# Kernel optimization log

Measured on AMD Instinct MI355X. Metric: run time of the kernel, lower is better.

## Reference

```python
import jax, jax.numpy as jnp
import numpy as np

K = 5            # dimW
PARAM_SIGMA = 0.08
LAMBDA_V = 2.0
C_MID = 192


def _conv5(x, w, b):
    # standard 5x5 SAME conv (the linear 'm' term of INRF)
    y = jax.lax.conv_general_dilated(x, w, (1, 1), 'SAME',
                                     dimension_numbers=('NCHW', 'OIHW', 'NCHW'))
    return y + b[None, :, None, None]


def _inrf(x, m_w, m_b, w_w):
    """INRF layer: out = (m * x) - lambda * sum_y w(y) sigma(x(y) - (g*x)(center)).
    dimG=1 so the Gaussian g*x is the identity (center pixel). The radiometric
    nonlinearity sigma is a saturating tanh with slope 1/paramSigma.
    """
    B, C, H, W = x.shape
    # windowed gather: [B, C*K*K, H, W], channel-major / spatial-minor ordering
    patches = jax.lax.conv_general_dilated_patches(x, (K, K), (1, 1), 'SAME')
    patches = patches.reshape(B, C, K * K, H, W)
    s = jnp.tanh((patches - x[:, :, None]) / PARAM_SIGMA)   # [B,C,KK,H,W]
    wterm = jnp.einsum('bckhw,ock->bohw', s, w_w)           # [B,Cout,H,W]
    return _conv5(x, m_w, m_b) - LAMBDA_V * wterm


def _maxpool2(x):
    return jax.lax.reduce_window(x, -jnp.inf, jax.lax.max,
                                 (1, 1, 2, 2), (1, 1, 2, 2), 'VALID')


def _avgpool8(x):
    s = jax.lax.reduce_window(x, 0.0, jax.lax.add,
                              (1, 1, 8, 8), (1, 1, 8, 8), 'VALID')
    return s / 64.0


def setup_inputs() -> dict:
    key = jax.random.key(0)
    ks = jax.random.split(key, 11)
    B = 64
    f32 = jnp.float32
    return {
        'x':    jax.random.normal(ks[0], (B, 3, 32, 32), f32),
        'm1_w': jax.random.normal(ks[1], (C_MID, 3, K, K), f32) * 0.05,
        'm1_b': jnp.zeros((C_MID,), f32),
        'w1_w': jax.random.normal(ks[2], (C_MID, 3, K * K), f32) * 0.05,
        'm2_w': jax.random.normal(ks[3], (C_MID, C_MID, K, K), f32) * 0.02,
        'm2_b': jnp.zeros((C_MID,), f32),
        'w2_w': jax.random.normal(ks[4], (C_MID, C_MID, K * K), f32) * 0.02,
        'm3_w': jax.random.normal(ks[5], (C_MID, C_MID, K, K), f32) * 0.02,
        'm3_b': jnp.zeros((C_MID,), f32),
        'w3_w': jax.random.normal(ks[6], (C_MID, C_MID, K * K), f32) * 0.02,
        'fc_w': jax.random.normal(ks[7], (10, C_MID), f32) * 0.05,
        'fc_b': jnp.zeros((10,), f32),
    }


def reference(x, m1_w, m1_b, w1_w, m2_w, m2_b, w2_w,
              m3_w, m3_b, w3_w, fc_w, fc_b):
    # dropout layers run in eval mode (identity); dp2d1 has p=0.0 anyway
    x00 = _maxpool2(_inrf(x, m1_w, m1_b, w1_w))      # [B,192,16,16]
    x01 = _inrf(x00, m2_w, m2_b, w2_w)               # [B,192,16,16]
    x03 = _maxpool2(x01)                             # [B,192,8,8]
    x04 = _inrf(x03, m3_w, m3_b, w3_w)               # [B,192,8,8]
    x05 = _avgpool8(x04)                             # [B,192,1,1]
    feat = x05.reshape(-1, C_MID)
    logits = feat @ fc_w.T + fc_b                    # [B,10]
    return (logits, x00, x01)
```

## Files before the change

kernel.cpp:

```cpp
#include <hip/hip_runtime.h>
#include <math.h>

#define COUT 192
#define NF 12

typedef __bf16 bf16_8 __attribute__((ext_vector_type(8)));
typedef float  f32x4  __attribute__((ext_vector_type(4)));

__device__ __forceinline__ float fast_tanh125(float d) {
    float e = __builtin_amdgcn_exp2f(d * 36.06737602222409f);
    return 1.0f - 2.0f * __builtin_amdgcn_rcpf(e + 1.0f);
}

__device__ __forceinline__ void gl_lds16(const void* gptr, void* lptr) {
    auto g = (const __attribute__((address_space(1))) unsigned int*)gptr;
    auto l = (__attribute__((address_space(3))) unsigned int*)lptr;
    __builtin_amdgcn_global_load_lds(g, l, 16, 0, 0);
}

#define BAR_VM4()  asm volatile("s_waitcnt vmcnt(4)\n\ts_barrier" ::: "memory")
#define BAR_VM3()  asm volatile("s_waitcnt vmcnt(3)\n\ts_barrier" ::: "memory")
#define BAR_VM0()  asm volatile("s_waitcnt vmcnt(0)\n\ts_barrier" ::: "memory")
#define BAR_VM4L() asm volatile("s_waitcnt vmcnt(4) lgkmcnt(0)\n\ts_barrier" ::: "memory")
#define BAR_VM3L() asm volatile("s_waitcnt vmcnt(3) lgkmcnt(0)\n\ts_barrier" ::: "memory")

__global__ void prep_all(const float* __restrict__ m1_w, const float* __restrict__ w1_w,
                         const float* __restrict__ m2_w, const float* __restrict__ w2_w,
                         const float* __restrict__ m3_w, const float* __restrict__ w3_w,
                         __bf16* __restrict__ Bp1, __bf16* __restrict__ Bp2,
                         __bf16* __restrict__ Bp3) {
    int idx = blockIdx.x * 256 + threadIdx.x;
    const int N1 = 3 * 2 * NF * 64, N2 = 192 * 2 * NF * 64;
    const float *mw, *ww; __bf16* Bp; int CIN, li;
    if (idx < N1)           { mw = m1_w; ww = w1_w; Bp = Bp1; CIN = 3;   li = idx; }
    else if (idx < N1 + N2) { mw = m2_w; ww = w2_w; Bp = Bp2; CIN = 192; li = idx - N1; }
    else if (idx < N1 + 2 * N2) { mw = m3_w; ww = w3_w; Bp = Bp3; CIN = 192; li = idx - N1 - N2; }
    else return;
    int lane = li & 63;
    int nf = (li >> 6) % NF;
    int cc = li / (NF * 64);
    int t = cc & 1, c = cc >> 1;
    int n = nf * 16 + (lane & 15);
    int k0 = (lane >> 4) * 8;
    bf16_8 v;
    #pragma unroll
    for (int e = 0; e < 8; ++e) {
        int k = k0 + e;
        float val = 0.f;
        if (k < 25) {
            val = (t == 0) ? mw[((size_t)n * CIN + c) * 25 + k]
                           : -2.0f * ww[((size_t)n * CIN + c) * 25 + k];
        }
        v[e] = (__bf16)val;
    }
    *(bf16_8*)(Bp + (size_t)li * 8) = v;
}

__global__ __launch_bounds__(256, 3) void inrf1_mfma(
    const float* __restrict__ x, const __bf16* __restrict__ Bp,
    const float* __restrict__ bias, float* __restrict__ x00)
{
    __shared__ float win[3][6][36];
    __shared__ float hp[192][33];

    const int b  = blockIdx.x >> 4;
    const int h0 = (blockIdx.x & 15) * 2;
    const int tid = threadIdx.x;
    const int wv = tid >> 6, lane = tid & 63;
    const int hl = wv >> 1, half = wv & 1;
    const int mcol = lane & 15, q = lane >> 4;
    const int wpos = half * 16 + mcol;

    for (int i = tid; i < 3 * 6 * 36; i += 256) {
        int c = i / 216, r = (i / 36) % 6, cc = i % 36;
        int gr = h0 + r - 2, gc = cc - 2;
        float v = 0.f;
        if (gr >= 0 && gr < 32 && gc >= 0 && gc < 32)
            v = x[((size_t)(b * 3 + c) * 32 + gr) * 32 + gc];
        win[c][r][cc] = v;
    }
    __syncthreads();

    int offs[8];
    #pragma unroll
    for (int e = 0; e < 8; ++e) {
        int k = q * 8 + e;
        int kk = (k < 25) ? k : 0;
        offs[e] = (hl + kk / 5) * 36 + wpos + (kk % 5);
    }
    const int cen_off = (hl + 2) * 36 + wpos + 2;

    f32x4 acc[NF];
    #pragma unroll
    for (int j = 0; j < NF; ++j) acc[j] = (f32x4){0.f, 0.f, 0.f, 0.f};

    const float* winf = &win[0][0][0];
    for (int c = 0; c < 3; ++c) {
        const float* wf = winf + c * 216;
        float cen = wf[cen_off];
        bf16_8 av, as_;
        #pragma unroll
        for (int e = 0; e < 8; ++e) {
            float v = wf[offs[e]];
            av[e] = (__bf16)v;
            as_[e] = (__bf16)fast_tanh125(v - cen);
        }
        const bf16_8* b0 = (const bf16_8*)Bp + ((size_t)(c * 2 + 0) * NF) * 64 + lane;
        const bf16_8* b1 = b0 + NF * 64;
        #pragma unroll
        for (int j = 0; j < NF; ++j)
            acc[j] = __builtin_amdgcn_mfma_f32_16x16x32_bf16(av, b0[j * 64], acc[j], 0, 0, 0);
        #pragma unroll
        for (int j = 0; j < NF; ++j)
            acc[j] = __builtin_amdgcn_mfma_f32_16x16x32_bf16(as_, b1[j * 64], acc[j], 0, 0, 0);
    }

    #pragma unroll
    for (int j = 0; j < NF; ++j) {
        int n = j * 16 + mcol;
        hp[n][hl * 16 + half * 8 + q * 2 + 0] = fmaxf(acc[j][0], acc[j][1]);
        hp[n][hl * 16 + half * 8 + q * 2 + 1] = fmaxf(acc[j][2], acc[j][3]);
    }
    __syncthreads();

    const int hpout = h0 >> 1;
    for (int i = tid; i < 192 * 16; i += 256) {
        int n = i >> 4, wp = i & 15;
        float v = fmaxf(hp[n][wp], hp[n][16 + wp]) + bias[n];
        x00[((size_t)(b * COUT + n) * 16 + hpout) * 16 + wp] = v;
    }
}

__global__ __launch_bounds__(512, 2) void inrf2_mfma(
    const float* __restrict__ xin, const __bf16* __restrict__ Bp,
    float* __restrict__ out0, float* __restrict__ part)
{
    constexpr int CPS = 48;
    __shared__ __align__(16) __bf16 Bs[3][24 * 64 * 8];
    __shared__ __align__(16) float slab[3][260];

    const int b  = blockIdx.x >> 2;
    const int ks = blockIdx.x & 3;
    const int c0 = ks * CPS;
    const int tid = threadIdx.x;
    const int wv = tid >> 6, lane = tid & 63;
    const int mg = wv & 3, nh = wv >> 2;
    const int wp = lane & 15, q = lane >> 4;

    int aoff[4][8];
    int cen_off[4];
    #pragma unroll
    for (int m = 0; m < 4; ++m) {
        const int crow = mg * 4 + m;
        cen_off[m] = crow * 16 + wp;
        #pragma unroll
        for (int e = 0; e < 8; ++e) {
            int kk = q * 8 + e;
            int dy = kk / 5 - 2, dx = kk % 5 - 2;
            int rr = crow + dy, cc2 = wp + dx;
            bool ok = (kk < 25) && (rr >= 0) && (rr < 16) && (cc2 >= 0) && (cc2 < 16);
            aoff[m][e] = ok ? (rr * 16 + cc2) : 256;
        }
    }

    const float* xb = xin + (size_t)b * COUT * 256;

    f32x4 acc[4][6];
    #pragma unroll
    for (int m = 0; m < 4; ++m)
        #pragma unroll
        for (int j = 0; j < 6; ++j) acc[m][j] = (f32x4){0.f, 0.f, 0.f, 0.f};

#define BUILD_A(SLOT, AV, AS)                                              \
    {                                                                      \
        const float* sb = slab[(SLOT)];                                    \
        _Pragma("unroll")                                                  \
        for (int m = 0; m < 4; ++m) {                                      \
            float cen = sb[cen_off[m]];                                    \
            _Pragma("unroll")                                              \
            for (int e = 0; e < 8; ++e) {                                  \
                float v = sb[aoff[m][e]];                                  \
                (AV)[m][e] = (__bf16)v;                                    \
                (AS)[m][e] = (__bf16)fast_tanh125(v - cen);                \
            }                                                              \
        }                                                                  \
    }

    if (tid < 12) slab[tid >> 2][256 + (tid & 3)] = 0.f;

    #pragma unroll
    for (int rr = 0; rr < 2; ++rr) {
        const int c = c0 + rr;
        if (wv == 0) gl_lds16(xb + (size_t)c * 256 + lane * 4, &slab[rr][0]);
        const __bf16* gB = Bp + (size_t)c * 12288 + wv * 1536 + lane * 8;
        #pragma unroll
        for (int i = 0; i < 3; ++i)
            gl_lds16(gB + i * 512, &Bs[rr][wv * 1536 + i * 512]);
    }
    if (wv == 0) { BAR_VM4L(); } else { BAR_VM3L(); }

    bf16_8 av[4], as_[4];

    #pragma unroll 3
    for (int r = 0; r < CPS; ++r) {
        const int sl_cur = r % 3;
        const int sl_n2  = (r + 2) % 3;
        const bool do2 = (r + 2) < CPS;

        if (do2) {
            const int c = c0 + r + 2;
            if (wv == 0) gl_lds16(xb + (size_t)c * 256 + lane * 4, &slab[sl_n2][0]);
            const __bf16* gB = Bp + (size_t)c * 12288 + wv * 1536 + lane * 8;
            #pragma unroll
            for (int i = 0; i < 3; ++i)
                gl_lds16(gB + i * 512, &Bs[sl_n2][wv * 1536 + i * 512]);
        }

        BUILD_A(sl_cur, av, as_);

        const bf16_8* Bf = (const bf16_8*)(Bs[sl_cur]) + lane;
        #pragma unroll
        for (int j = 0; j < 6; ++j) {
            bf16_8 fm = Bf[(nh * 6 + j) * 64];
            bf16_8 fs = Bf[(12 + nh * 6 + j) * 64];
            #pragma unroll
            for (int m = 0; m < 4; ++m) {
                acc[m][j] = __builtin_amdgcn_mfma_f32_16x16x32_bf16(av[m],  fm, acc[m][j], 0, 0, 0);
                acc[m][j] = __builtin_amdgcn_mfma_f32_16x16x32_bf16(as_[m], fs, acc[m][j], 0, 0, 0);
            }
        }

        if (do2) {
            if (wv == 0) { BAR_VM4(); } else { BAR_VM3(); }
        } else {
            BAR_VM0();
        }
    }
#undef BUILD_A

    float* outp = (ks == 0) ? out0 : (part + (size_t)(ks - 1) * 3145728);
    #pragma unroll
    for (int j = 0; j < 6; ++j) {
        int n = (nh * 6 + j) * 16 + wp;
        #pragma unroll
        for (int m = 0; m < 4; ++m) {
            int h = mg * 4 + m;
            *(f32x4*)&outp[((size_t)(b * COUT + n)) * 256 + h * 16 + q * 4] = acc[m][j];
        }
    }
}

__global__ __launch_bounds__(512) void finish2(
    float* __restrict__ x01, const float* __restrict__ part,
    const float* __restrict__ bias, __bf16* __restrict__ An)
{
    __shared__ float xbuf[8][256];
    const int b  = blockIdx.x / 24;
    const int cg = blockIdx.x % 24;
    const int tid = threadIdx.x;
    const int wv = tid >> 6, lane = tid & 63;
    const int ch = cg * 8 + wv;

    float* p0 = x01 + ((size_t)b * COUT + ch) * 256;
    const float* pp = part + ((size_t)b * COUT + ch) * 256;
    const float bv = bias[ch];
    #pragma unroll
    for (int i = 0; i < 4; ++i) {
        int idx = lane + 64 * i;
        float s = ((p0[idx] + pp[idx]) + pp[idx + 3145728]) + pp[idx + 2 * 3145728] + bv;
        xbuf[wv][idx] = s;
        p0[idx] = s;
    }
    __syncthreads();

    const int ph = lane >> 3, pw = lane & 7;
    const int i0 = ph * 32 + pw * 2;
    float x8 = fmaxf(fmaxf(xbuf[wv][i0], xbuf[wv][i0 + 1]),
                     fmaxf(xbuf[wv][i0 + 16], xbuf[wv][i0 + 17]));

    float myT = 0.f, myW = 0.f;
    #pragma unroll
    for (int k = 0; k < 25; ++k) {
        const int dy = k / 5 - 2, dx = k % 5 - 2;
        const bool valid = (ph + dy >= 0) && (ph + dy < 8) && (pw + dx >= 0) && (pw + dx < 8);
        float nb = __shfl(x8, (lane + dy * 8 + dx) & 63);
        nb = valid ? nb : 0.f;
        float tS = fast_tanh125(nb - x8);
        float wS = nb;
        #pragma unroll
        for (int off = 1; off < 64; off <<= 1) {
            tS += __shfl_xor(tS, off);
            wS += __shfl_xor(wS, off);
        }
        if (lane == k) { myT = tS; myW = wS; }
    }

    const int mt = b >> 4;
    if (lane < 25) {
        const int k = lane;
        const int la = (k >> 3) * 16 + (b & 15);
        const int e = k & 7;
        const int ccW = ch * 2, ccT = ch * 2 + 1;
        An[((size_t)(ccW * 4 + mt) * 64 + la) * 8 + e] = (__bf16)(myW * 0.015625f);
        An[((size_t)(ccT * 4 + mt) * 64 + la) * 8 + e] = (__bf16)(myT * 0.015625f);
    } else if (lane < 32) {
        const int la = 3 * 16 + (b & 15);
        const int e = lane & 7;
        const int ccW = ch * 2, ccT = ch * 2 + 1;
        An[((size_t)(ccW * 4 + mt) * 64 + la) * 8 + e] = (__bf16)0.f;
        An[((size_t)(ccT * 4 + mt) * 64 + la) * 8 + e] = (__bf16)0.f;
    }
}

__global__ __launch_bounds__(512) void gemm3p(
    const __bf16* __restrict__ An, const __bf16* __restrict__ Bp,
    float* __restrict__ part)
{
    const int ks = blockIdx.x;
    const int tid = threadIdx.x;
    const int wv = tid >> 6, lane = tid & 63;
    const int mt = wv & 3, nh = wv >> 2;

    f32x4 acc[6];
    #pragma unroll
    for (int j = 0; j < 6; ++j) acc[j] = (f32x4){0.f, 0.f, 0.f, 0.f};

    for (int i = 0; i < 4; ++i) {
        const int cc = ks * 4 + i;
        bf16_8 a = *(const bf16_8*)(An + ((size_t)(cc * 4 + mt) * 64 + lane) * 8);
        #pragma unroll
        for (int j = 0; j < 6; ++j) {
            bf16_8 bw = *(const bf16_8*)(Bp + ((size_t)(cc * NF + nh * 6 + j) * 64 + lane) * 8);
            acc[j] = __builtin_amdgcn_mfma_f32_16x16x32_bf16(a, bw, acc[j], 0, 0, 0);
        }
    }
    #pragma unroll
    for (int j = 0; j < 6; ++j) {
        int n = (nh * 6 + j) * 16 + (lane & 15);
        *(f32x4*)(part + ((size_t)ks * COUT + n) * 64 + mt * 16 + (lane >> 4) * 4) = acc[j];
    }
}

__global__ __launch_bounds__(256) void logitsk(
    const float* __restrict__ part, const float* __restrict__ m3_b,
    const float* __restrict__ fc_w, const float* __restrict__ fc_b,
    float* __restrict__ logits)
{
    __shared__ float feat[COUT];
    const int b = blockIdx.x;
    const int t = threadIdx.x;
    if (t < COUT) {
        float s = 0.f;
        for (int ks = 0; ks < 96; ++ks) s += part[((size_t)ks * COUT + t) * 64 + b];
        feat[t] = s + m3_b[t];
    }
    __syncthreads();
    if (t < 10) {
        float s = fc_b[t];
        #pragma unroll 8
        for (int c = 0; c < COUT; ++c) s = fmaf(fc_w[t * COUT + c], feat[c], s);
        logits[(size_t)b * 10 + t] = s;
    }
}

extern "C" void kernel_launch(void* const* d_in, const int* in_sizes, int n_in,
                              void* d_out, int out_size, void* d_ws, size_t ws_size,
                              hipStream_t stream) {
    const float* x    = (const float*)d_in[0];
    const float* m1_w = (const float*)d_in[1];
    const float* m1_b = (const float*)d_in[2];
    const float* w1_w = (const float*)d_in[3];
    const float* m2_w = (const float*)d_in[4];
    const float* m2_b = (const float*)d_in[5];
    const float* w2_w = (const float*)d_in[6];
    const float* m3_w = (const float*)d_in[7];
    const float* m3_b = (const float*)d_in[8];
    const float* w3_w = (const float*)d_in[9];
    const float* fc_w = (const float*)d_in[10];
    const float* fc_b = (const float*)d_in[11];

    float* out = (float*)d_out;
    float* ws  = (float*)d_ws;

    float* logits = out;
    float* x00 = out + 640;
    float* x01 = out + 640 + 3145728;

    __bf16* Bp1  = (__bf16*)(ws);
    __bf16* Bp2  = (__bf16*)(ws + 18432);
    __bf16* Bp3  = (__bf16*)(ws + 1198080);
    __bf16* An   = (__bf16*)(ws + 2377728);
    float*  part2 = ws + 2770944;
    float*  part3 = ws + 2770944;

    prep_all<<<2322, 256, 0, stream>>>(m1_w, w1_w, m2_w, w2_w, m3_w, w3_w, Bp1, Bp2, Bp3);

    inrf1_mfma<<<64 * 16, 256, 0, stream>>>(x, Bp1, m1_b, x00);
    inrf2_mfma<<<64 * 4, 512, 0, stream>>>(x00, Bp2, x01, part2);
    finish2<<<64 * 24, 512, 0, stream>>>(x01, part2, m2_b, An);
    gemm3p<<<96, 512, 0, stream>>>(An, Bp3, part3);
    logitsk<<<64, 256, 0, stream>>>(part3, m3_b, fc_w, fc_b, logits);
}
```

Measured before the change: 230.2 us.

## Feed inrf2 from a zero-padded global x00 copy via direct register loads

inrf1 now also writes x00 into a zero-padded 20x20 per-channel buffer, which prep_all zero-fills beforehand. inrf2 no longer stages each input channel slab through LDS. Each lane instead gathers its 5x5 window values straight from global memory into registers, double-buffered one channel ahead, with no bounds checks thanks to the padding. This removes LDS slab traffic and the per-channel vmcnt/lgkmcnt waits, at the cost of extra global writes, a large zero-fill and many redundant global loads that rely on the cache. The B-weight triple buffering stays, but the explicit vmcnt waits before each barrier are gone, so correctness now depends on implicit load completion.

New measurement: 231.0 us. Within noise of the previous version (+0.4%).

```diff
diff --git a/kernel.cpp b/kernel.cpp
--- a/kernel.cpp
+++ b/kernel.cpp
@@ -18,24 +18,23 @@
     __builtin_amdgcn_global_load_lds(g, l, 16, 0, 0);
 }
 
-#define BAR_VM4()  asm volatile("s_waitcnt vmcnt(4)\n\ts_barrier" ::: "memory")
-#define BAR_VM3()  asm volatile("s_waitcnt vmcnt(3)\n\ts_barrier" ::: "memory")
-#define BAR_VM0()  asm volatile("s_waitcnt vmcnt(0)\n\ts_barrier" ::: "memory")
-#define BAR_VM4L() asm volatile("s_waitcnt vmcnt(4) lgkmcnt(0)\n\ts_barrier" ::: "memory")
-#define BAR_VM3L() asm volatile("s_waitcnt vmcnt(3) lgkmcnt(0)\n\ts_barrier" ::: "memory")
-
 __global__ void prep_all(const float* __restrict__ m1_w, const float* __restrict__ w1_w,
                          const float* __restrict__ m2_w, const float* __restrict__ w2_w,
                          const float* __restrict__ m3_w, const float* __restrict__ w3_w,
                          __bf16* __restrict__ Bp1, __bf16* __restrict__ Bp2,
-                         __bf16* __restrict__ Bp3) {
+                         __bf16* __restrict__ Bp3, float* __restrict__ x00p) {
     int idx = blockIdx.x * 256 + threadIdx.x;
     const int N1 = 3 * 2 * NF * 64, N2 = 192 * 2 * NF * 64;
+    const int NW = N1 + 2 * N2;
+    if (idx >= NW) {
+        int zi = idx - NW;
+        if (zi < 1228800) ((f32x4*)x00p)[zi] = (f32x4){0.f, 0.f, 0.f, 0.f};
+        return;
+    }
     const float *mw, *ww; __bf16* Bp; int CIN, li;
     if (idx < N1)           { mw = m1_w; ww = w1_w; Bp = Bp1; CIN = 3;   li = idx; }
     else if (idx < N1 + N2) { mw = m2_w; ww = w2_w; Bp = Bp2; CIN = 192; li = idx - N1; }
-    else if (idx < N1 + 2 * N2) { mw = m3_w; ww = w3_w; Bp = Bp3; CIN = 192; li = idx - N1 - N2; }
-    else return;
+    else                    { mw = m3_w; ww = w3_w; Bp = Bp3; CIN = 192; li = idx - N1 - N2; }
     int lane = li & 63;
     int nf = (li >> 6) % NF;
     int cc = li / (NF * 64);
@@ -58,7 +57,8 @@
 
 __global__ __launch_bounds__(256, 3) void inrf1_mfma(
     const float* __restrict__ x, const __bf16* __restrict__ Bp,
-    const float* __restrict__ bias, float* __restrict__ x00)
+    const float* __restrict__ bias, float* __restrict__ x00,
+    float* __restrict__ x00p)
 {
     __shared__ float win[3][6][36];
     __shared__ float hp[192][33];
@@ -128,16 +128,16 @@
         int n = i >> 4, wp = i & 15;
         float v = fmaxf(hp[n][wp], hp[n][16 + wp]) + bias[n];
         x00[((size_t)(b * COUT + n) * 16 + hpout) * 16 + wp] = v;
+        x00p[(size_t)(b * COUT + n) * 400 + (hpout + 2) * 20 + (wp + 2)] = v;
     }
 }
 
 __global__ __launch_bounds__(512, 2) void inrf2_mfma(
-    const float* __restrict__ xin, const __bf16* __restrict__ Bp,
+    const float* __restrict__ x00p, const __bf16* __restrict__ Bp,
     float* __restrict__ out0, float* __restrict__ part)
 {
     constexpr int CPS = 48;
     __shared__ __align__(16) __bf16 Bs[3][24 * 64 * 8];
-    __shared__ __align__(16) float slab[3][260];
 
     const int b  = blockIdx.x >> 2;
     const int ks = blockIdx.x & 3;
@@ -147,23 +147,17 @@
     const int mg = wv & 3, nh = wv >> 2;
     const int wp = lane & 15, q = lane >> 4;
 
-    int aoff[4][8];
-    int cen_off[4];
-    #pragma unroll
-    for (int m = 0; m < 4; ++m) {
-        const int crow = mg * 4 + m;
-        cen_off[m] = crow * 16 + wp;
-        #pragma unroll
-        for (int e = 0; e < 8; ++e) {
-            int kk = q * 8 + e;
-            int dy = kk / 5 - 2, dx = kk % 5 - 2;
-            int rr = crow + dy, cc2 = wp + dx;
-            bool ok = (kk < 25) && (rr >= 0) && (rr < 16) && (cc2 >= 0) && (cc2 < 16);
-            aoff[m][e] = ok ? (rr * 16 + cc2) : 256;
-        }
-    }
-
-    const float* xb = xin + (size_t)b * COUT * 256;
+    int goff[9];
+    #pragma unroll
+    for (int e = 0; e < 8; ++e) {
+        int kk = q * 8 + e;
+        int k2 = (kk < 25) ? kk : 12;
+        int dy = k2 / 5 - 2, dx = k2 % 5 - 2;
+        goff[e] = (mg * 4 + dy + 2) * 20 + (wp + dx + 2);
+    }
+    goff[8] = (mg * 4 + 2) * 20 + (wp + 2);
+
+    const float* xs = x00p + (size_t)(b * COUT + c0) * 400;
 
     f32x4 acc[4][6];
     #pragma unroll
@@ -171,72 +165,70 @@
         #pragma unroll
         for (int j = 0; j < 6; ++j) acc[m][j] = (f32x4){0.f, 0.f, 0.f, 0.f};
 
-#define BUILD_A(SLOT, AV, AS)                                              \
+#define ISSUE_B(c, slot)                                                   \
     {                                                                      \
-        const float* sb = slab[(SLOT)];                                    \
+        const __bf16* gB = Bp + (size_t)(c) * 12288 + wv * 1536 + lane * 8;\
+        _Pragma("unroll")                                                  \
+        for (int i = 0; i < 3; ++i)                                        \
+            gl_lds16(gB + i * 512, &Bs[(slot)][wv * 1536 + i * 512]);      \
+    }
+
+#define LOAD_A(c, DST)                                                     \
+    {                                                                      \
+        const float* xc = xs + (size_t)(c) * 400;                          \
         _Pragma("unroll")                                                  \
         for (int m = 0; m < 4; ++m) {                                      \
-            float cen = sb[cen_off[m]];                                    \
+            _Pragma("unroll")                                              \
+            for (int i = 0; i < 9; ++i)                                    \
+                (DST)[m][i] = xc[goff[i] + m * 20];                        \
+        }                                                                  \
+    }
+
+#define STEP(r, CUR, NXT)                                                  \
+    {                                                                      \
+        const int sl_cur = (r) % 3;                                        \
+        if ((r) + 2 < CPS) ISSUE_B(c0 + (r) + 2, ((r) + 2) % 3);           \
+        if ((r) + 1 < CPS) LOAD_A((r) + 1, NXT);                           \
+        bf16_8 av[4], as_[4];                                              \
+        _Pragma("unroll")                                                  \
+        for (int m = 0; m < 4; ++m) {                                      \
+            float cen = (CUR)[m][8];                                       \
             _Pragma("unroll")                                              \
             for (int e = 0; e < 8; ++e) {                                  \
-                float v = sb[aoff[m][e]];                                  \
-                (AV)[m][e] = (__bf16)v;                                    \
-                (AS)[m][e] = (__bf16)fast_tanh125(v - cen);                \
+                float v = (CUR)[m][e];                                     \
+                av[m][e] = (__bf16)v;                                      \
+                as_[m][e] = (__bf16)fast_tanh125(v - cen);                 \
             }                                                              \
         }                                                                  \
-    }
-
-    if (tid < 12) slab[tid >> 2][256 + (tid & 3)] = 0.f;
-
-    #pragma unroll
-    for (int rr = 0; rr < 2; ++rr) {
-        const int c = c0 + rr;
-        if (wv == 0) gl_lds16(xb + (size_t)c * 256 + lane * 4, &slab[rr][0]);
-        const __bf16* gB = Bp + (size_t)c * 12288 + wv * 1536 + lane * 8;
-        #pragma unroll
-        for (int i = 0; i < 3; ++i)
-            gl_lds16(gB + i * 512, &Bs[rr][wv * 1536 + i * 512]);
-    }
-    if (wv == 0) { BAR_VM4L(); } else { BAR_VM3L(); }
-
-    bf16_8 av[4], as_[4];
-
-    #pragma unroll 3
-    for (int r = 0; r < CPS; ++r) {
-        const int sl_cur = r % 3;
-        const int sl_n2  = (r + 2) % 3;
-        const bool do2 = (r + 2) < CPS;
-
-        if (do2) {
-            const int c = c0 + r + 2;
-            if (wv == 0) gl_lds16(xb + (size_t)c * 256 + lane * 4, &slab[sl_n2][0]);
-            const __bf16* gB = Bp + (size_t)c * 12288 + wv * 1536 + lane * 8;
-            #pragma unroll
-            for (int i = 0; i < 3; ++i)
-                gl_lds16(gB + i * 512, &Bs[sl_n2][wv * 1536 + i * 512]);
-        }
-
-        BUILD_A(sl_cur, av, as_);
-
-        const bf16_8* Bf = (const bf16_8*)(Bs[sl_cur]) + lane;
-        #pragma unroll
-        for (int j = 0; j < 6; ++j) {
-            bf16_8 fm = Bf[(nh * 6 + j) * 64];
-            bf16_8 fs = Bf[(12 + nh * 6 + j) * 64];
-            #pragma unroll
-            for (int m = 0; m < 4; ++m) {
-                acc[m][j] = __builtin_amdgcn_mfma_f32_16x16x32_bf16(av[m],  fm, acc[m][j], 0, 0, 0);
-                acc[m][j] = __builtin_amdgcn_mfma_f32_16x16x32_bf16(as_[m], fs, acc[m][j], 0, 0, 0);
-            }
-        }
-
-        if (do2) {
-            if (wv == 0) { BAR_VM4(); } else { BAR_VM3(); }
-        } else {
-            BAR_VM0();
-        }
-    }
-#undef BUILD_A
+        const bf16_8* Bf = (const bf16_8*)(Bs[sl_cur]) + lane;             \
+        _Pragma("unroll")                                                  \
+        for (int j = 0; j < 6; ++j) {                                      \
+            bf16_8 fm = Bf[(nh * 6 + j) * 64];                             \
+            bf16_8 fs = Bf[(12 + nh * 6 + j) * 64];                        \
+            _Pragma("unroll")                                              \
+            for (int m = 0; m < 4; ++m) {                                  \
+                acc[m][j] = __builtin_amdgcn_mfma_f32_16x16x32_bf16(av[m],  fm, acc[m][j], 0, 0, 0); \
+                acc[m][j] = __builtin_amdgcn_mfma_f32_16x16x32_bf16(as_[m], fs, acc[m][j], 0, 0, 0); \
+            }                                                              \
+        }                                                                  \
+        __builtin_amdgcn_s_barrier();                                      \
+    }
+
+    float arawA[4][9], arawB[4][9];
+
+    ISSUE_B(c0, 0);
+    asm volatile("s_waitcnt vmcnt(0)" ::: "memory");
+    __builtin_amdgcn_s_barrier();
+    ISSUE_B(c0 + 1, 1);
+    LOAD_A(0, arawA);
+
+    for (int r2 = 0; r2 < CPS / 2; ++r2) {
+        STEP(2 * r2,     arawA, arawB);
+        STEP(2 * r2 + 1, arawB, arawA);
+    }
+#undef STEP
+#undef LOAD_A
+#undef ISSUE_B
 
     float* outp = (ks == 0) ? out0 : (part + (size_t)(ks - 1) * 3145728);
     #pragma unroll
@@ -392,11 +384,13 @@
     __bf16* An   = (__bf16*)(ws + 2377728);
     float*  part2 = ws + 2770944;
     float*  part3 = ws + 2770944;
-
-    prep_all<<<2322, 256, 0, stream>>>(m1_w, w1_w, m2_w, w2_w, m3_w, w3_w, Bp1, Bp2, Bp3);
-
-    inrf1_mfma<<<64 * 16, 256, 0, stream>>>(x, Bp1, m1_b, x00);
-    inrf2_mfma<<<64 * 4, 512, 0, stream>>>(x00, Bp2, x01, part2);
+    float*  x00p  = ws + 12208128;
+
+    prep_all<<<7122, 256, 0, stream>>>(m1_w, w1_w, m2_w, w2_w, m3_w, w3_w,
+                                       Bp1, Bp2, Bp3, x00p);
+
+    inrf1_mfma<<<64 * 16, 256, 0, stream>>>(x, Bp1, m1_b, x00, x00p);
+    inrf2_mfma<<<64 * 4, 512, 0, stream>>>(x00p, Bp2, x01, part2);
     finish2<<<64 * 24, 512, 0, stream>>>(x01, part2, m2_b, An);
     gemm3p<<<96, 512, 0, stream>>>(An, Bp3, part3);
     logitsk<<<64, 256, 0, stream>>>(part3, m3_b, fc_w, fc_b, logits);
```
